# Kernel tuning notes

Measured on AMD Instinct MI355X. Metric: run time of the kernel, lower is better.

## Reference

```python
import jax, jax.numpy as jnp
import numpy as np

TOP_K = 2

def setup_inputs() -> dict:
    key = jax.random.key(0)
    ks = jax.random.split(key, 5)
    B, T, C, E, H = 4, 2048, 1024, 16, 4096
    x = jax.random.normal(ks[0], (B, T, C), dtype=jnp.float32)
    w_router = jax.random.normal(ks[1], (C, E), dtype=jnp.float32) / np.sqrt(C)
    w1 = jax.random.normal(ks[2], (E, C, H), dtype=jnp.float32) / np.sqrt(C)
    b1 = jnp.zeros((E, H), dtype=jnp.float32)
    w2 = jax.random.normal(ks[3], (E, H, C), dtype=jnp.float32) / np.sqrt(H)
    b2 = jnp.zeros((E, C), dtype=jnp.float32)
    return {"x": x, "w_router": w_router, "w1": w1, "b1": b1, "w2": w2, "b2": b2}


def reference(x, w_router, w1, b1, w2, b2):
    B, T, C = x.shape
    E = w1.shape[0]
    xf = x.reshape(-1, C)                       # [N, C]
    N = xf.shape[0]

    logits = xf @ w_router                      # [N, E]
    rw, sel = jax.lax.top_k(logits, TOP_K)      # [N, K]
    rw = jax.nn.softmax(rw.astype(jnp.float32), axis=-1).astype(x.dtype)

    # combine weight per (token, expert): sum of routing weights over the
    # k-slots that selected that expert (equivalent to the per-k masked loop)
    comb = jnp.zeros((N, E), dtype=x.dtype)
    comb = comb.at[jnp.arange(N)[:, None], sel].add(rw)  # [N, E]

    # loop over experts via scan: out += comb[:, e:e+1] * FFN_e(xf)
    def step(acc, params):
        w1e, b1e, w2e, b2e, ce = params         # ce: [N]
        h = jax.nn.relu(xf @ w1e + b1e)         # [N, 4C]
        y = h @ w2e + b2e                       # [N, C]
        return acc + ce[:, None] * y, None

    out0 = jnp.zeros_like(xf)
    out, _ = jax.lax.scan(step, out0, (w1, b1, w2, b2, comb.T))
    return out.reshape(B, T, C)
```

## Files before the change

### kernel.cpp

```cpp
#include <hip/hip_runtime.h>
#include <hip/hip_bf16.h>


typedef __attribute__((ext_vector_type(4))) float f32x4;
typedef __attribute__((ext_vector_type(8))) __bf16 bf16x8;
typedef __attribute__((ext_vector_type(8))) unsigned short u16x8;

#define NEXP 16
#define CAP  2048
#define CDIM 1024
#define HDIM 4096
#define BM 128
#define BN 128
#define BK 64

__device__ __forceinline__ unsigned short f2bf(float f) {
  return __builtin_bit_cast(unsigned short, (__bf16)f);
}

__device__ __forceinline__ int swz(int row, int b) {
  return row * (BK * 2) + (b ^ (((row >> 1) & 7) << 4));
}

typedef __attribute__((address_space(3))) void  lds_void;
typedef __attribute__((address_space(1))) const void gbl_void;
__device__ __forceinline__ void gload16(const void* g, void* l) {
  __builtin_amdgcn_global_load_lds((gbl_void*)g, (lds_void*)l, 16, 0, 0);
}

__global__ __launch_bounds__(64) void router_kernel(
    const float* __restrict__ x, const float* __restrict__ wr,
    float* __restrict__ pair_w, int* __restrict__ counts,
    int* __restrict__ lists)
{
  const int n = blockIdx.x;
  const int l = threadIdx.x;
  const float* xrow = x + (size_t)n * CDIM;
  double acc[NEXP];
#pragma unroll
  for (int e = 0; e < NEXP; e++) acc[e] = 0.0;
  for (int it = 0; it < CDIM / 64; it++) {
    const int c = l + it * 64;
    const double xv = (double)xrow[c];
    const float* w = wr + c * NEXP;
#pragma unroll
    for (int e = 0; e < NEXP; e++) acc[e] += xv * (double)w[e];
  }
#pragma unroll
  for (int e = 0; e < NEXP; e++) {
    double v = acc[e];
    for (int off = 32; off > 0; off >>= 1) v += __shfl_xor(v, off, 64);
    acc[e] = v;
  }
  if (l == 0) {
    int e0 = 0; double b0 = acc[0];
    for (int e = 1; e < NEXP; e++) if (acc[e] > b0) { b0 = acc[e]; e0 = e; }
    int e1 = -1; double b1v = -1e300;
    for (int e = 0; e < NEXP; e++) {
      if (e == e0) continue;
      if (acc[e] > b1v) { b1v = acc[e]; e1 = e; }
    }
    const double d = exp(b1v - b0);
    pair_w[2 * n]     = (float)(1.0 / (1.0 + d));
    pair_w[2 * n + 1] = (float)(d / (1.0 + d));
    int p0 = atomicAdd(&counts[e0], 1);
    if (p0 < CAP) lists[e0 * CAP + p0] = 2 * n;
    int p1 = atomicAdd(&counts[e1], 1);
    if (p1 < CAP) lists[e1 * CAP + p1] = 2 * n + 1;
  }
}

__global__ __launch_bounds__(256) void cvt_x_kernel(
    const float* __restrict__ x, unsigned short* __restrict__ xb, int n8)
{
  const int i = blockIdx.x * 256 + threadIdx.x;
  if (i >= n8) return;
  float4 a = ((const float4*)x)[2 * i];
  float4 b = ((const float4*)x)[2 * i + 1];
  u16x8 v;
  v[0] = f2bf(a.x); v[1] = f2bf(a.y); v[2] = f2bf(a.z); v[3] = f2bf(a.w);
  v[4] = f2bf(b.x); v[5] = f2bf(b.y); v[6] = f2bf(b.z); v[7] = f2bf(b.w);
  ((u16x8*)xb)[i] = v;
}

__global__ __launch_bounds__(256) void transpose_cvt_kernel(
    const float* __restrict__ src, unsigned short* __restrict__ dst,
    int K, int Nn)
{
  __shared__ __align__(16) unsigned short tile[64][72];
  const size_t eoff = (size_t)blockIdx.z * K * Nn;
  const float* S = src + eoff;
  unsigned short* D = dst + eoff;
  const int n0 = blockIdx.x * 64, k0 = blockIdx.y * 64;
  const int t = threadIdx.x;
  {
    const int nl = (t & 15) * 4, kr = t >> 4;
#pragma unroll
    for (int p = 0; p < 4; p++) {
      const int k = kr + p * 16;
      float4 v = *(const float4*)(S + (size_t)(k0 + k) * Nn + n0 + nl);
      tile[nl + 0][k] = f2bf(v.x);
      tile[nl + 1][k] = f2bf(v.y);
      tile[nl + 2][k] = f2bf(v.z);
      tile[nl + 3][k] = f2bf(v.w);
    }
  }
  __syncthreads();
  {
    const int kq = (t & 7) * 8, nr = t >> 3;
#pragma unroll
    for (int p = 0; p < 2; p++) {
      const int n = nr + p * 32;
      u16x8 v = *(const u16x8*)&tile[n][kq];
      *(u16x8*)(D + (size_t)(n0 + n) * K + k0 + kq) = v;
    }
  }
}

__global__ __launch_bounds__(256) void gemm1_async_kernel(
    const unsigned short* __restrict__ xb, const unsigned short* __restrict__ wb,
    const float* __restrict__ b1, const int* __restrict__ counts,
    const int* __restrict__ lists, unsigned short* __restrict__ Hb)
{
  const int e = blockIdx.z;
  int cnt = counts[e]; if (cnt > CAP) cnt = CAP;
  const int m0 = blockIdx.y * BM;
  if (m0 >= cnt) return;
  const int n0 = blockIdx.x * BN;
  const int* list = lists + e * CAP;
  const unsigned short* W = wb + (size_t)e * CDIM * HDIM;

  __shared__ __align__(16) unsigned short As[BM * BK];
  __shared__ __align__(16) unsigned short Bs[BN * BK];

  const int t = threadIdx.x, wid = t >> 6, lane = t & 63;
  const char* ag[4]; const char* bg[4];
  unsigned short* al[4]; unsigned short* bl[4];
#pragma unroll
  for (int i = 0; i < 4; i++) {
    const int r = wid * 32 + i * 8 + (lane >> 3);
    const int cb = ((lane & 7) ^ ((r >> 1) & 7)) << 4;
    int ai = m0 + r; if (ai > cnt - 1) ai = cnt - 1;
    const int tok = list[ai] >> 1;
    ag[i] = (const char*)(xb + (size_t)tok * CDIM) + cb;
    bg[i] = (const char*)(W + (size_t)(n0 + r) * CDIM) + cb;
    al[i] = As + (wid * 32 + i * 8) * BK;
    bl[i] = Bs + (wid * 32 + i * 8) * BK;
  }

  const int wm = (wid >> 1) * 64, wn = (wid & 1) * 64;
  const int lrow = lane & 15, lgrp = lane >> 4;
  f32x4 acc[4][4] = {};

  for (int kt = 0; kt < CDIM; kt += BK) {
#pragma unroll
    for (int i = 0; i < 4; i++) {
      gload16(ag[i] + kt * 2, al[i]);
      gload16(bg[i] + kt * 2, bl[i]);
    }
    __syncthreads();
#pragma unroll
    for (int kk = 0; kk < 2; kk++) {
      bf16x8 af[4], bfr[4];
      const int kb = (kk * 32 + lgrp * 8) * 2;
#pragma unroll
      for (int i = 0; i < 4; i++)
        af[i] = *(const bf16x8*)((const char*)As + swz(wm + i * 16 + lrow, kb));
#pragma unroll
      for (int j = 0; j < 4; j++)
        bfr[j] = *(const bf16x8*)((const char*)Bs + swz(wn + j * 16 + lrow, kb));
#pragma unroll
      for (int i = 0; i < 4; i++)
#pragma unroll
        for (int j = 0; j < 4; j++)
          acc[i][j] = __builtin_amdgcn_mfma_f32_16x16x32_bf16(af[i], bfr[j], acc[i][j], 0, 0, 0);
    }
    __syncthreads();
  }

  int hrow[4][4]; bool valid[4][4];
#pragma unroll
  for (int i = 0; i < 4; i++)
#pragma unroll
    for (int r = 0; r < 4; r++) {
      const int mi = m0 + wm + i * 16 + lgrp * 4 + r;
      valid[i][r] = (mi < cnt);
      hrow[i][r] = list[valid[i][r] ? mi : (cnt - 1)];
    }
#pragma unroll
  for (int j = 0; j < 4; j++) {
    const int col = n0 + wn + j * 16 + lrow;
    const float bias = b1[e * HDIM + col];
#pragma unroll
    for (int i = 0; i < 4; i++)
#pragma unroll
      for (int r = 0; r < 4; r++)
        if (valid[i][r]) {
          float h = acc[i][j][r] + bias;
          h = h > 0.f ? h : 0.f;
          Hb[(size_t)hrow[i][r] * HDIM + col] = f2bf(h);
        }
  }
}

__global__ __launch_bounds__(256) void gemm2_async_kernel(
    const unsigned short* __restrict__ Hb, const unsigned short* __restrict__ wb,
    const float* __restrict__ b2, const float* __restrict__ pair_w,
    const int* __restrict__ counts, const int* __restrict__ lists,
    float* __restrict__ out)
{
  const int e = blockIdx.z;
  int cnt = counts[e]; if (cnt > CAP) cnt = CAP;
  const int m0 = blockIdx.y * BM;
  if (m0 >= cnt) return;
  const int n0 = blockIdx.x * BN;
  const int* list = lists + e * CAP;
  const unsigned short* W = wb + (size_t)e * HDIM * CDIM;

  __shared__ __align__(16) unsigned short As[BM * BK];
  __shared__ __align__(16) unsigned short Bs[BN * BK];

  const int t = threadIdx.x, wid = t >> 6, lane = t & 63;
  const char* ag[4]; const char* bg[4];
  unsigned short* al[4]; unsigned short* bl[4];
#pragma unroll
  for (int i = 0; i < 4; i++) {
    const int r = wid * 32 + i * 8 + (lane >> 3);
    const int cb = ((lane & 7) ^ ((r >> 1) & 7)) << 4;
    int ai = m0 + r; if (ai > cnt - 1) ai = cnt - 1;
    const int pr = list[ai];
    ag[i] = (const char*)(Hb + (size_t)pr * HDIM) + cb;
    bg[i] = (const char*)(W + (size_t)(n0 + r) * HDIM) + cb;
    al[i] = As + (wid * 32 + i * 8) * BK;
    bl[i] = Bs + (wid * 32 + i * 8) * BK;
  }

  const int wm = (wid >> 1) * 64, wn = (wid & 1) * 64;
  const int lrow = lane & 15, lgrp = lane >> 4;
  f32x4 acc[4][4] = {};

  for (int kt = 0; kt < HDIM; kt += BK) {
#pragma unroll
    for (int i = 0; i < 4; i++) {
      gload16(ag[i] + kt * 2, al[i]);
      gload16(bg[i] + kt * 2, bl[i]);
    }
    __syncthreads();
#pragma unroll
    for (int kk = 0; kk < 2; kk++) {
      bf16x8 af[4], bfr[4];
      const int kb = (kk * 32 + lgrp * 8) * 2;
#pragma unroll
      for (int i = 0; i < 4; i++)
        af[i] = *(const bf16x8*)((const char*)As + swz(wm + i * 16 + lrow, kb));
#pragma unroll
      for (int j = 0; j < 4; j++)
        bfr[j] = *(const bf16x8*)((const char*)Bs + swz(wn + j * 16 + lrow, kb));
#pragma unroll
      for (int i = 0; i < 4; i++)
#pragma unroll
        for (int j = 0; j < 4; j++)
          acc[i][j] = __builtin_amdgcn_mfma_f32_16x16x32_bf16(af[i], bfr[j], acc[i][j], 0, 0, 0);
    }
    __syncthreads();
  }

  float wgt[4][4]; int tok[4][4]; bool valid[4][4];
#pragma unroll
  for (int i = 0; i < 4; i++)
#pragma unroll
    for (int r = 0; r < 4; r++) {
      const int mi = m0 + wm + i * 16 + lgrp * 4 + r;
      valid[i][r] = (mi < cnt);
      const int p = list[valid[i][r] ? mi : (cnt - 1)];
      wgt[i][r] = pair_w[p];
      tok[i][r] = p >> 1;
    }
#pragma unroll
  for (int j = 0; j < 4; j++) {
    const int col = n0 + wn + j * 16 + lrow;
    const float bias = b2[e * CDIM + col];
#pragma unroll
    for (int i = 0; i < 4; i++)
#pragma unroll
      for (int r = 0; r < 4; r++)
        if (valid[i][r])
          atomicAdd(out + (size_t)tok[i][r] * CDIM + col,
                    wgt[i][r] * (acc[i][j][r] + bias));
  }
}

__global__ __launch_bounds__(256) void gemm1_f32_kernel(
    const float* __restrict__ x, const float* __restrict__ w1,
    const float* __restrict__ b1, const int* __restrict__ counts,
    const int* __restrict__ lists, unsigned short* __restrict__ Hb,
    int e_base, int h_by_pair)
{
  const int e = e_base + blockIdx.z;
  int cnt = counts[e]; if (cnt > CAP) cnt = CAP;
  const int m0 = blockIdx.y * BM;
  if (m0 >= cnt) return;
  const int n0 = blockIdx.x * BN;
  const int* list = lists + e * CAP;
  const float* W = w1 + (size_t)e * CDIM * HDIM;
  __shared__ __align__(16) unsigned short As[BM * BK];
  __shared__ __align__(16) unsigned short Bs[BN * BK];
  const int t = threadIdx.x;
  const int a_row = t >> 1, a_half = t & 1;
  int a_idx = m0 + a_row; if (a_idx > cnt - 1) a_idx = cnt - 1;
  const float* a_src = x + (size_t)(list[a_idx] >> 1) * CDIM + a_half * 32;
  const int b_np = t & 63, b_kg = t >> 6;
  const int wid = t >> 6, lane = t & 63;
  const int wm = (wid >> 1) * 64, wn = (wid & 1) * 64;
  const int lrow = lane & 15, lgrp = lane >> 4;
  f32x4 acc[4][4] = {};
  for (int kt = 0; kt < CDIM; kt += BK) {
    {
      const float* s = a_src + kt;
      u16x8 cv[4];
#pragma unroll
      for (int q = 0; q < 4; q++) {
        float4 v0 = *(const float4*)(s + q * 8);
        float4 v1 = *(const float4*)(s + q * 8 + 4);
        cv[q][0] = f2bf(v0.x); cv[q][1] = f2bf(v0.y);
        cv[q][2] = f2bf(v0.z); cv[q][3] = f2bf(v0.w);
        cv[q][4] = f2bf(v1.x); cv[q][5] = f2bf(v1.y);
        cv[q][6] = f2bf(v1.z); cv[q][7] = f2bf(v1.w);
      }
#pragma unroll
      for (int q = 0; q < 4; q++)
        *(u16x8*)((char*)As + swz(a_row, (a_half * 32 + q * 8) * 2)) = cv[q];
    }
    {
#pragma unroll
      for (int it = 0; it < 2; it++) {
        const int k0 = (b_kg + 4 * it) * 8;
        u16x8 c0, c1;
#pragma unroll
        for (int j = 0; j < 8; j++) {
          float2 v = *(const float2*)(W + (size_t)(kt + k0 + j) * HDIM + n0 + 2 * b_np);
          c0[j] = f2bf(v.x); c1[j] = f2bf(v.y);
        }
        *(u16x8*)((char*)Bs + swz(2 * b_np,     k0 * 2)) = c0;
        *(u16x8*)((char*)Bs + swz(2 * b_np + 1, k0 * 2)) = c1;
      }
    }
    __syncthreads();
#pragma unroll
    for (int kk = 0; kk < 2; kk++) {
      bf16x8 af[4], bfr[4];
      const int kb = (kk * 32 + lgrp * 8) * 2;
#pragma unroll
      for (int i = 0; i < 4; i++)
        af[i] = *(const bf16x8*)((const char*)As + swz(wm + i * 16 + lrow, kb));
#pragma unroll
      for (int j = 0; j < 4; j++)
        bfr[j] = *(const bf16x8*)((const char*)Bs + swz(wn + j * 16 + lrow, kb));
#pragma unroll
      for (int i = 0; i < 4; i++)
#pragma unroll
        for (int j = 0; j < 4; j++)
          acc[i][j] = __builtin_amdgcn_mfma_f32_16x16x32_bf16(af[i], bfr[j], acc[i][j], 0, 0, 0);
    }
    __syncthreads();
  }
  int hrow[4][4]; bool valid[4][4];
#pragma unroll
  for (int i = 0; i < 4; i++)
#pragma unroll
    for (int r = 0; r < 4; r++) {
      const int mi = m0 + wm + i * 16 + lgrp * 4 + r;
      valid[i][r] = (mi < cnt);
      const int idx = valid[i][r] ? mi : (cnt - 1);
      hrow[i][r] = h_by_pair ? list[idx] : idx;
    }
#pragma unroll
  for (int j = 0; j < 4; j++) {
    const int col = n0 + wn + j * 16 + lrow;
    const float bias = b1[e * HDIM + col];
#pragma unroll
    for (int i = 0; i < 4; i++)
#pragma unroll
      for (int r = 0; r < 4; r++)
        if (valid[i][r]) {
          float h = acc[i][j][r] + bias;
          h = h > 0.f ? h : 0.f;
          Hb[(size_t)hrow[i][r] * HDIM + col] = f2bf(h);
        }
  }
}

__global__ __launch_bounds__(256) void gemm2_f32_kernel(
    const unsigned short* __restrict__ Hb, const float* __restrict__ w2,
    const float* __restrict__ b2, const float* __restrict__ pair_w,
    const int* __restrict__ counts, const int* __restrict__ lists,
    float* __restrict__ out, int e_base, int h_by_pair)
{
  const int e = e_base + blockIdx.z;
  int cnt = counts[e]; if (cnt > CAP) cnt = CAP;
  const int m0 = blockIdx.y * BM;
  if (m0 >= cnt) return;
  const int n0 = blockIdx.x * BN;
  const int* list = lists + e * CAP;
  const float* W = w2 + (size_t)e * HDIM * CDIM;
  __shared__ __align__(16) unsigned short As[BM * BK];
  __shared__ __align__(16) unsigned short Bs[BN * BK];
  const int t = threadIdx.x;
  const int a_row = t >> 1, a_half = t & 1;
  int a_idx = m0 + a_row; if (a_idx > cnt - 1) a_idx = cnt - 1;
  const unsigned short* a_src =
      Hb + (size_t)(h_by_pair ? list[a_idx] : a_idx) * HDIM + a_half * 32;
  const int b_np = t & 63, b_kg = t >> 6;
  const int wid = t >> 6, lane = t & 63;
  const int wm = (wid >> 1) * 64, wn = (wid & 1) * 64;
  const int lrow = lane & 15, lgrp = lane >> 4;
  f32x4 acc[4][4] = {};
  for (int kt = 0; kt < HDIM; kt += BK) {
    {
      const unsigned short* s = a_src + kt;
#pragma unroll
      for (int q = 0; q < 4; q++) {
        u16x8 v = *(const u16x8*)(s + q * 8);
        *(u16x8*)((char*)As + swz(a_row, (a_half * 32 + q * 8) * 2)) = v;
      }
    }
    {
#pragma unroll
      for (int it = 0; it < 2; it++) {
        const int k0 = (b_kg + 4 * it) * 8;
        u16x8 c0, c1;
#pragma unroll
        for (int j = 0; j < 8; j++) {
          float2 v = *(const float2*)(W + (size_t)(kt + k0 + j) * CDIM + n0 + 2 * b_np);
          c0[j] = f2bf(v.x); c1[j] = f2bf(v.y);
        }
        *(u16x8*)((char*)Bs + swz(2 * b_np,     k0 * 2)) = c0;
        *(u16x8*)((char*)Bs + swz(2 * b_np + 1, k0 * 2)) = c1;
      }
    }
    __syncthreads();
#pragma unroll
    for (int kk = 0; kk < 2; kk++) {
      bf16x8 af[4], bfr[4];
      const int kb = (kk * 32 + lgrp * 8) * 2;
#pragma unroll
      for (int i = 0; i < 4; i++)
        af[i] = *(const bf16x8*)((const char*)As + swz(wm + i * 16 + lrow, kb));
#pragma unroll
      for (int j = 0; j < 4; j++)
        bfr[j] = *(const bf16x8*)((const char*)Bs + swz(wn + j * 16 + lrow, kb));
#pragma unroll
      for (int i = 0; i < 4; i++)
#pragma unroll
        for (int j = 0; j < 4; j++)
          acc[i][j] = __builtin_amdgcn_mfma_f32_16x16x32_bf16(af[i], bfr[j], acc[i][j], 0, 0, 0);
    }
    __syncthreads();
  }
  float wgt[4][4]; int tok[4][4]; bool valid[4][4];
#pragma unroll
  for (int i = 0; i < 4; i++)
#pragma unroll
    for (int r = 0; r < 4; r++) {
      const int mi = m0 + wm + i * 16 + lgrp * 4 + r;
      valid[i][r] = (mi < cnt);
      const int idx = valid[i][r] ? mi : (cnt - 1);
      const int p = list[idx];
      wgt[i][r] = pair_w[p];
      tok[i][r] = p >> 1;
    }
#pragma unroll
  for (int j = 0; j < 4; j++) {
    const int col = n0 + wn + j * 16 + lrow;
    const float bias = b2[e * CDIM + col];
#pragma unroll
    for (int i = 0; i < 4; i++)
#pragma unroll
      for (int r = 0; r < 4; r++)
        if (valid[i][r])
          atomicAdd(out + (size_t)tok[i][r] * CDIM + col,
                    wgt[i][r] * (acc[i][j][r] + bias));
  }
}

extern "C" void kernel_launch(void* const* d_in, const int* in_sizes, int n_in,
                              void* d_out, int out_size, void* d_ws, size_t ws_size,
                              hipStream_t stream)
{
  const float* x  = (const float*)d_in[0];
  const float* wr = (const float*)d_in[1];
  const float* w1 = (const float*)d_in[2];
  const float* b1 = (const float*)d_in[3];
  const float* w2 = (const float*)d_in[4];
  const float* b2 = (const float*)d_in[5];
  float* out = (float*)d_out;

  const int N = in_sizes[0] / CDIM;

  char* ws = (char*)d_ws;
  int* counts = (int*)ws;
  int* lists  = (int*)(ws + 256);
  float* pw   = (float*)(ws + 256 + NEXP * CAP * 4);
  size_t off = 256 + (size_t)NEXP * CAP * 4 + (size_t)2 * N * 4;
  off = (off + 255) & ~(size_t)255;
  unsigned short* xb = (unsigned short*)(ws + off);
  const size_t xb_sz = (size_t)N * CDIM * 2;
  unsigned short* Hb = (unsigned short*)(ws + off + xb_sz);
  const size_t Hb_sz = (size_t)2 * N * HDIM * 2;
  unsigned short* wb = (unsigned short*)(ws + off + xb_sz + Hb_sz);
  const size_t wb_sz = (size_t)NEXP * CDIM * HDIM * 2;

  const size_t need_new = off + xb_sz + Hb_sz + wb_sz;
  const size_t need_old = off + Hb_sz;

  hipMemsetAsync(d_ws, 0, 64, stream);
  hipMemsetAsync(d_out, 0, (size_t)out_size * 4, stream);

  router_kernel<<<N, 64, 0, stream>>>(x, wr, pw, counts, lists);

  if (ws_size >= need_new) {
    cvt_x_kernel<<<(N * CDIM / 8 + 255) / 256, 256, 0, stream>>>(
        x, xb, N * CDIM / 8);
    transpose_cvt_kernel<<<dim3(HDIM / 64, CDIM / 64, NEXP), 256, 0, stream>>>(
        w1, wb, CDIM, HDIM);
    gemm1_async_kernel<<<dim3(HDIM / BN, CAP / BM, NEXP), 256, 0, stream>>>(
        xb, wb, b1, counts, lists, Hb);
    transpose_cvt_kernel<<<dim3(CDIM / 64, HDIM / 64, NEXP), 256, 0, stream>>>(
        w2, wb, HDIM, CDIM);
    gemm2_async_kernel<<<dim3(CDIM / BN, CAP / BM, NEXP), 256, 0, stream>>>(
        Hb, wb, b2, pw, counts, lists, out);
  } else if (ws_size >= need_old) {
    unsigned short* Hb0 = (unsigned short*)(ws + off);
    gemm1_f32_kernel<<<dim3(HDIM / BN, CAP / BM, NEXP), 256, 0, stream>>>(
        x, w1, b1, counts, lists, Hb0, 0, 1);
    gemm2_f32_kernel<<<dim3(CDIM / BN, CAP / BM, NEXP), 256, 0, stream>>>(
        Hb0, w2, b2, pw, counts, lists, out, 0, 1);
  }
}
```

Before: 1.085 ms.

## Split-K gemm2 across two halves and remap workgroups across XCDs

Adds an XCD-aware block remapping to both grouped GEMM kernels so that consecutive logical tiles land on the same XCD, which is meant to improve L2 reuse of weights and tokens. gemm2 is also split along K into two halves, doubling its grid so more CUs have work when per-expert token counts are small. Partial sums are combined through the existing atomicAdd, and the bias is added only by the first split. The cost is twice as many atomic writes to the output, and the remap assumes the workgroup count divides evenly by 8.

```diff
diff --git a/kernel.cpp b/kernel.cpp
--- a/kernel.cpp
+++ b/kernel.cpp
@@ -13,6 +13,7 @@
 #define BM 128
 #define BN 128
 #define BK 64
+#define KS2 2
 
 __device__ __forceinline__ unsigned short f2bf(float f) {
   return __builtin_bit_cast(unsigned short, (__bf16)f);
@@ -26,6 +27,17 @@
 typedef __attribute__((address_space(1))) const void gbl_void;
 __device__ __forceinline__ void gload16(const void* g, void* l) {
   __builtin_amdgcn_global_load_lds((gbl_void*)g, (lds_void*)l, 16, 0, 0);
+}
+
+__device__ __forceinline__ void xcd_remap(int& bx, int& by, int& bz) {
+  const int gx = gridDim.x, gy = gridDim.y;
+  const int nwg = gx * gy * gridDim.z;
+  int flat = blockIdx.x + gx * (blockIdx.y + gy * blockIdx.z);
+  flat = (flat & 7) * (nwg >> 3) + (flat >> 3);
+  bx = flat % gx;
+  const int t = flat / gx;
+  by = t % gy;
+  bz = t / gy;
 }
 
 __global__ __launch_bounds__(64) void router_kernel(
@@ -122,11 +134,13 @@
     const float* __restrict__ b1, const int* __restrict__ counts,
     const int* __restrict__ lists, unsigned short* __restrict__ Hb)
 {
-  const int e = blockIdx.z;
+  int bx, by, bz;
+  xcd_remap(bx, by, bz);
+  const int e = bz;
   int cnt = counts[e]; if (cnt > CAP) cnt = CAP;
-  const int m0 = blockIdx.y * BM;
+  const int m0 = by * BM;
   if (m0 >= cnt) return;
-  const int n0 = blockIdx.x * BN;
+  const int n0 = bx * BN;
   const int* list = lists + e * CAP;
   const unsigned short* W = wb + (size_t)e * CDIM * HDIM;
 
@@ -209,13 +223,16 @@
     const int* __restrict__ counts, const int* __restrict__ lists,
     float* __restrict__ out)
 {
-  const int e = blockIdx.z;
+  int bx, by, bz;
+  xcd_remap(bx, by, bz);
+  const int e = bz / KS2, ks = bz % KS2;
   int cnt = counts[e]; if (cnt > CAP) cnt = CAP;
-  const int m0 = blockIdx.y * BM;
+  const int m0 = by * BM;
   if (m0 >= cnt) return;
-  const int n0 = blockIdx.x * BN;
+  const int n0 = bx * BN;
   const int* list = lists + e * CAP;
   const unsigned short* W = wb + (size_t)e * HDIM * CDIM;
+  const int kbeg = ks * (HDIM / KS2), kend = kbeg + HDIM / KS2;
 
   __shared__ __align__(16) unsigned short As[BM * BK];
   __shared__ __align__(16) unsigned short Bs[BN * BK];
@@ -239,7 +256,7 @@
   const int lrow = lane & 15, lgrp = lane >> 4;
   f32x4 acc[4][4] = {};
 
-  for (int kt = 0; kt < HDIM; kt += BK) {
+  for (int kt = kbeg; kt < kend; kt += BK) {
 #pragma unroll
     for (int i = 0; i < 4; i++) {
       gload16(ag[i] + kt * 2, al[i]);
@@ -279,7 +296,7 @@
 #pragma unroll
   for (int j = 0; j < 4; j++) {
     const int col = n0 + wn + j * 16 + lrow;
-    const float bias = b2[e * CDIM + col];
+    const float bias = (ks == 0) ? b2[e * CDIM + col] : 0.f;
 #pragma unroll
     for (int i = 0; i < 4; i++)
 #pragma unroll
@@ -527,7 +544,7 @@
         xb, wb, b1, counts, lists, Hb);
     transpose_cvt_kernel<<<dim3(CDIM / 64, HDIM / 64, NEXP), 256, 0, stream>>>(
         w2, wb, HDIM, CDIM);
-    gemm2_async_kernel<<<dim3(CDIM / BN, CAP / BM, NEXP), 256, 0, stream>>>(
+    gemm2_async_kernel<<<dim3(CDIM / BN, CAP / BM, NEXP * KS2), 256, 0, stream>>>(
         Hb, wb, b2, pw, counts, lists, out);
   } else if (ws_size >= need_old) {
     unsigned short* Hb0 = (unsigned short*)(ws + off);
```

New measurement: 1.088 ms. No clear change (+0.3%).
